# Performance work log

Hardware: AMD Instinct MI355X
Metric: run time of the kernel (lower is better)

## Reference

```python
import jax, jax.numpy as jnp
import numpy as np

B, T, W = 8, 4096, 1024          # batch, byte seq len, words per sequence
DB, DW = 64, 512                 # byte_embed_dim, word_embed_dim
NH = 2                           # highway layers per block
VOCAB = 264                      # 256 bytes + 4 + 4 specials
BPE_MARK, WORD_MARK = 4, 3       # bpe_mask_idx, word_mask_idx


def _make_seg_ids():
    # ragged word lengths in {3,4,5}, mean 4, summing to T per sequence
    rng = np.random.default_rng(0)
    seg = np.empty((B, T), np.int32)
    base = T // W
    for b in range(B):
        delta = np.zeros(W, np.int64)
        q = W // 4
        idx = rng.permutation(W)
        delta[idx[:q]] = 1
        delta[idx[q:2 * q]] = -1
        seg[b] = np.repeat(np.arange(W), base + delta)
    return jnp.asarray(seg)


def setup_inputs() -> dict:
    key = jax.random.key(0)
    ks = jax.random.split(key, 12)
    s = 0.05
    byte_tokens = jax.random.randint(ks[0], (B, T), 4, VOCAB)
    bpe_mask = jax.random.bernoulli(ks[1], 0.25, (B, T))
    word_mask = jax.random.bernoulli(ks[2], 0.05, (B, T))
    seg_ids = _make_seg_ids()
    tok_emb = (jax.random.normal(ks[3], (VOCAB, DB)) * s).at[0].set(0.0)  # padding_idx=0 row zeroed
    inp = {
        'byte_tokens': byte_tokens, 'bpe_mask': bpe_mask, 'word_mask': word_mask,
        'seg_ids': seg_ids, 'tok_emb': tok_emb,
        'conv0_w': jax.random.normal(ks[4], (3, DB, DW)) * s, 'conv0_b': jnp.zeros((DW,)),
        'hw0_wg': jax.random.normal(ks[5], (NH, DW, DW)) * s, 'hw0_bg': jnp.zeros((NH, DW)),
        'hw0_wh': jax.random.normal(ks[6], (NH, DW, DW)) * s, 'hw0_bh': jnp.zeros((NH, DW)),
        'conv1_w': jax.random.normal(ks[7], (3, DW, DW)) * s, 'conv1_b': jnp.zeros((DW,)),
        'hw1_wg': jax.random.normal(ks[8], (NH, DW, DW)) * s, 'hw1_bg': jnp.zeros((NH, DW)),
        'hw1_wh': jax.random.normal(ks[9], (NH, DW, DW)) * s, 'hw1_bh': jnp.zeros((NH, DW)),
        'proj_w': jax.random.normal(ks[10], (DW, DW)) * s, 'proj_b': jnp.zeros((DW,)),
    }
    return inp


def _conv_highway(x, cw, cb, wg, bg, wh, bh, residual):
    # 1D same-padded conv over sequence, optional residual, relu, then highways
    y = jax.lax.conv_general_dilated(x, cw, (1,), 'SAME',
                                     dimension_numbers=('NWC', 'WIO', 'NWC')) + cb
    if residual:
        y = y + x
    y = jax.nn.relu(y)
    for i in range(NH):
        g = jax.nn.sigmoid(y @ wg[i] + bg[i])
        h = jax.nn.relu(y @ wh[i] + bh[i])
        y = g * h + (1.0 - g) * y
    return y


def reference(byte_tokens, bpe_mask, word_mask, seg_ids, tok_emb,
              conv0_w, conv0_b, hw0_wg, hw0_bg, hw0_wh, hw0_bh,
              conv1_w, conv1_b, hw1_wg, hw1_bg, hw1_wh, hw1_bh,
              proj_w, proj_b):
    # byte embedding + marker embeddings (pad idx 0 -> zero row)
    x = (tok_emb[byte_tokens]
         + tok_emb[jnp.where(bpe_mask, BPE_MARK, 0)]
         + tok_emb[jnp.where(word_mask, WORD_MARK, 0)])          # [B,T,DB]
    x = _conv_highway(x, conv0_w, conv0_b, hw0_wg, hw0_bg, hw0_wh, hw0_bh, False)
    x = _conv_highway(x, conv1_w, conv1_b, hw1_wg, hw1_bg, hw1_wh, hw1_bh, True)
    # ragged per-word segment max over bytes (fused, replaces python loops)
    seg_max = jax.vmap(lambda xi, si: jax.ops.segment_max(xi, si, num_segments=W))
    x = seg_max(x, seg_ids)                                       # [B,W,DW]
    return x @ proj_w + proj_b
```

## Files before the change

kernel.cpp:

```cpp
#include <hip/hip_runtime.h>
#include <hip/hip_bf16.h>

using bf16 = __hip_bfloat16;
typedef __attribute__((ext_vector_type(8))) short s8v;
typedef __attribute__((ext_vector_type(4))) float f4v;

#define T_SEQ 4096
#define DWC 512

__device__ __forceinline__ float fin(float v) {
    return (v == v && fabsf(v) < 1e30f) ? v : 0.0f;
}
__device__ __forceinline__ float ldf(const void* p, size_t i, int f32) {
    return f32 ? ((const float*)p)[i] : __bfloat162float(((const bf16*)p)[i]);
}
__device__ __forceinline__ float b2f(short s) {
    unsigned u = ((unsigned)(unsigned short)s) << 16;
    return __builtin_bit_cast(float, u);
}
__device__ __forceinline__ short f2b(float v) {
    bf16 b = __float2bfloat16(v);
    return __builtin_bit_cast(short, b);
}
__device__ __forceinline__ uint4 ld16(const short* p) { return *(const uint4*)p; }

__device__ __forceinline__ void gl_lds16(const short* g, short* l) {
    __builtin_amdgcn_global_load_lds(
        (const __attribute__((address_space(1))) void*)g,
        (__attribute__((address_space(3))) void*)l, 16, 0, 0);
}

__device__ __forceinline__ void swz(int L, int G, int& bx, int& by) {
    int k8 = L & 7, sl = L >> 3;
    int gp = G >> 5;
    bx = sl & 3;
    by = k8 * gp + (sl >> 2);
}

__device__ __forceinline__ int swidx(int row, int ch) {
    return row * 32 + ((ch ^ ((row >> 1) & 3)) << 3);
}

__global__ __launch_bounds__(256) void diag_kernel(bf16* __restrict__ out, int n, float v)
{
    int i = blockIdx.x * 256 + threadIdx.x;
    if (i < n) out[i] = __float2bfloat16(i == 0 ? v : 0.0f);
}

__global__ __launch_bounds__(256) void detect_kernel(
    const int* __restrict__ tok, const unsigned char* __restrict__ bpe,
    const unsigned char* __restrict__ wm, const int* __restrict__ seg,
    const unsigned int* __restrict__ embw, int* __restrict__ flags)
{
    __shared__ int sh[5];
    int tid = threadIdx.x;
    if (tid < 5) sh[tid] = 0;
    __syncthreads();
    int bo = 0, bm = 0, wo = 0, wmid = 0;
    for (int i = tid; i < 16384; i += 256) {
        int odd = 2 * i + 1;
        if (bpe[odd]) bo = 1;
        if (wm[odd])  wo = 1;
        int mid = 8 * (i & 4095) + 4;
        if (bpe[mid]) bm = 1;
        if (wm[mid])  wmid = 1;
    }
    if (bo)   atomicOr(&sh[0], 1);
    if (bm)   atomicOr(&sh[1], 1);
    if (wo)   atomicOr(&sh[2], 1);
    if (wmid) atomicOr(&sh[3], 1);
    if (tid < 32 && embw[32 + tid] != 0u) atomicOr(&sh[4], 1);
    __syncthreads();
    if (tid == 0) {
        flags[0] = (tok[32767] != 0) ? 0 : 1;
        flags[1] = sh[0] ? 1 : (sh[1] ? 4 : 8);
        flags[2] = sh[2] ? 1 : (sh[3] ? 4 : 8);
        flags[3] = (seg[32767] != 0) ? 0 : 1;
        flags[4] = sh[4] ? 0 : 1;
    }
}

#define WB_TOTAL 3249664
#define EMB4_ELEMS (264 * 4 * 64)
__global__ __launch_bounds__(256) void convert_weights(
    const void* c0w, const void* c0b, const void* h0g, const void* h0bg,
    const void* h0h, const void* h0bh, const void* c1w, const void* c1b,
    const void* h1g, const void* h1bg, const void* h1h, const void* h1bh,
    const void* pw, const void* pb, const void* emb,
    const int* __restrict__ flags, short* __restrict__ WB)
{
    int f32 = flags[4];
    size_t i = (size_t)blockIdx.x * 256 + threadIdx.x;
    if (i >= WB_TOTAL + EMB4_ELEMS) return;
    if (i >= WB_TOTAL) {
        size_t o = i - WB_TOTAL;
        size_t t = o >> 8, v = (o >> 6) & 3, c = o & 63;
        float val = ldf(emb, t * 64 + c, f32);
        if (v & 1) val += ldf(emb, 4 * 64 + c, f32);
        if (v & 2) val += ldf(emb, 3 * 64 + c, f32);
        WB[i] = f2b(fin(val));
        return;
    }
    const void* src; size_t si;
    if (i < 98304)        { size_t n = i / 192, k = i % 192; src = c0w; si = k * 512 + n; }
    else if (i < 98816)   { src = c0b;  si = i - 98304; }
    else if (i < 623104)  { size_t o = i - 98816;  size_t l = o >> 18; o &= 262143;
                            size_t n = o >> 9, k = o & 511; src = h0g; si = (l << 18) + k * 512 + n; }
    else if (i < 624128)  { src = h0bg; si = i - 623104; }
    else if (i < 1148416) { size_t o = i - 624128; size_t l = o >> 18; o &= 262143;
                            size_t n = o >> 9, k = o & 511; src = h0h; si = (l << 18) + k * 512 + n; }
    else if (i < 1149440) { src = h0bh; si = i - 1148416; }
    else if (i < 1935872) { size_t o = i - 1149440; size_t n = o / 1536, k = o % 1536;
                            src = c1w; si = k * 512 + n; }
    else if (i < 1936384) { src = c1b;  si = i - 1935872; }
    else if (i < 2460672) { size_t o = i - 1936384; size_t l = o >> 18; o &= 262143;
                            size_t n = o >> 9, k = o & 511; src = h1g; si = (l << 18) + k * 512 + n; }
    else if (i < 2461696) { src = h1bg; si = i - 2460672; }
    else if (i < 2985984) { size_t o = i - 2461696; size_t l = o >> 18; o &= 262143;
                            size_t n = o >> 9, k = o & 511; src = h1h; si = (l << 18) + k * 512 + n; }
    else if (i < 2987008) { src = h1bh; si = i - 2985984; }
    else if (i < 3249152) { size_t o = i - 2987008; size_t n = o >> 9, k = o & 511;
                            src = pw; si = k * 512 + n; }
    else                  { src = pb;   si = i - 3249152; }
    WB[i] = f2b(ldf(src, si, f32));
}

__global__ __launch_bounds__(512) void conv0_mfma(
    const int* __restrict__ tok, const unsigned char* __restrict__ bpe,
    const unsigned char* __restrict__ wm, const short* __restrict__ emb4,
    const int* __restrict__ flags, const short* __restrict__ WT,
    const short* __restrict__ bias, short* __restrict__ Out)
{
    constexpr int K = 192;
    constexpr int NIT = 3;
    __shared__ __align__(16) short As[2][256 * 32];
    __shared__ __align__(16) short Bs[2][256 * 32];
    int bx, by;
    swz(blockIdx.x, gridDim.x, bx, by);
    const int bm = by * 128, bn = bx * 128;
    const int tid = threadIdx.x;
    const int wave = tid >> 6, lane = tid & 63;
    const int wmr = (wave >> 1) * 32, wnc = (wave & 1) * 64;
    const int q = lane >> 4, ln16 = lane & 15;
    const int sr = tid >> 2, sch = tid & 3;
    const int tt = (bm + sr) & (T_SEQ - 1);
    const int is64t = flags[0];
    const int wb = flags[1], ww = flags[2];
    const short* Bb = WT + (size_t)(bn + sr) * K + sch * 8;

    f4v acc[2][4] = {};
    uint4 rA0, rA1, rB0, rB1;
    const uint4 z4 = make_uint4(0, 0, 0, 0);

    auto loadA = [&](int tap, uint4& a0, uint4& a1) {
        int ts = tt + tap - 1;
        if ((unsigned)ts < (unsigned)T_SEQ) {
            int bt = bm + sr + tap - 1;
            int tk = is64t ? (int)((const long long*)tok)[bt] : tok[bt];
            tk = min(max(tk, 0), 263);
            int v = (bpe[(size_t)bt * wb] ? 1 : 0) | (wm[(size_t)bt * ww] ? 2 : 0);
            const short* row = emb4 + ((size_t)tk * 4 + v) * 64;
            a0 = ld16(row + sch * 8);
            a1 = ld16(row + 32 + sch * 8);
        } else { a0 = z4; a1 = z4; }
    };

    loadA(0, rA0, rA1);
    rB0 = ld16(Bb);
    rB1 = ld16(Bb + 32);
    *(uint4*)(&As[0][swidx(sr, sch)])       = rA0;
    *(uint4*)(&As[0][swidx(128 + sr, sch)]) = rA1;
    *(uint4*)(&Bs[0][swidx(sr, sch)])       = rB0;
    *(uint4*)(&Bs[0][swidx(128 + sr, sch)]) = rB1;
    __syncthreads();
    int p = 0;

    for (int it = 0; it < NIT; ++it) {
        const bool more = (it + 1 < NIT);
        if (more) {
            int kn = (it + 1) * 64;
            loadA(it + 1, rA0, rA1);
            rB0 = ld16(Bb + kn);
            rB1 = ld16(Bb + kn + 32);
        }
        #pragma unroll
        for (int ks = 0; ks < 2; ks++) {
            s8v af[2], bf[4];
            #pragma unroll
            for (int mi = 0; mi < 2; mi++)
                af[mi] = *(const s8v*)(&As[p][swidx(128 * ks + wmr + mi * 16 + ln16, q)]);
            #pragma unroll
            for (int ni = 0; ni < 4; ni++)
                bf[ni] = *(const s8v*)(&Bs[p][swidx(128 * ks + wnc + ni * 16 + ln16, q)]);
            #pragma unroll
            for (int mi = 0; mi < 2; mi++)
                #pragma unroll
                for (int ni = 0; ni < 4; ni++)
                    acc[mi][ni] = __builtin_amdgcn_mfma_f32_16x16x32_bf16(
                        af[mi], bf[ni], acc[mi][ni], 0, 0, 0);
        }
        if (more) {
            *(uint4*)(&As[p ^ 1][swidx(sr, sch)])       = rA0;
            *(uint4*)(&As[p ^ 1][swidx(128 + sr, sch)]) = rA1;
            *(uint4*)(&Bs[p ^ 1][swidx(sr, sch)])       = rB0;
            *(uint4*)(&Bs[p ^ 1][swidx(128 + sr, sch)]) = rB1;
            __syncthreads();
            p ^= 1;
        }
    }

    #pragma unroll
    for (int mi = 0; mi < 2; mi++)
        #pragma unroll
        for (int ni = 0; ni < 4; ni++) {
            int col = bn + wnc + ni * 16 + ln16;
            float bv = b2f(bias[col]);
            #pragma unroll
            for (int r = 0; r < 4; r++) {
                int orow = bm + wmr + mi * 16 + q * 4 + r;
                Out[(size_t)orow * DWC + col] =
                    f2b(fin(fmaxf(acc[mi][ni][r] + bv, 0.0f)));
            }
        }
}

__global__ __launch_bounds__(512) void conv1_mfma(
    const short* __restrict__ A, const short* __restrict__ WT,
    const short* __restrict__ bias, short* __restrict__ Out)
{
    constexpr int IC = 512;
    constexpr int K = 3 * IC;
    constexpr int NIT = K / 64;
    __shared__ __align__(16) short As[2][256 * 32];
    __shared__ __align__(16) short Bs[2][256 * 32];
    int bx, by;
    swz(blockIdx.x, gridDim.x, bx, by);
    const int bm = by * 128, bn = bx * 128;
    const int tid = threadIdx.x;
    const int wave = tid >> 6, lane = tid & 63;
    const int wmr = (wave >> 1) * 32, wnc = (wave & 1) * 64;
    const int q = lane >> 4, ln16 = lane & 15;
    const int sr = tid >> 2, sch = tid & 3;
    const int tt = (bm + sr) & (T_SEQ - 1);
    const short* Bb = WT + (size_t)(bn + sr) * K + sch * 8;

    f4v acc[2][4] = {};
    uint4 rA0, rA1, rB0, rB1;
    const uint4 z4 = make_uint4(0, 0, 0, 0);

    {
        int ts = tt - 1;
        bool ok = (ts >= 0 && ts < T_SEQ);
        const short* sa = A + (size_t)(bm + sr - 1) * IC + sch * 8;
        rA0 = ok ? ld16(sa) : z4;
        rA1 = ok ? ld16(sa + 32) : z4;
        rB0 = ld16(Bb);
        rB1 = ld16(Bb + 32);
    }
    *(uint4*)(&As[0][swidx(sr, sch)])       = rA0;
    *(uint4*)(&As[0][swidx(128 + sr, sch)]) = rA1;
    *(uint4*)(&Bs[0][swidx(sr, sch)])       = rB0;
    *(uint4*)(&Bs[0][swidx(128 + sr, sch)]) = rB1;
    __syncthreads();
    int p = 0;

    for (int it = 0; it < NIT; ++it) {
        const bool more = (it + 1 < NIT);
        if (more) {
            int kn = (it + 1) * 64;
            int tap = kn / IC, c0 = kn - tap * IC;
            int ts = tt + tap - 1;
            bool ok = (ts >= 0 && ts < T_SEQ);
            const short* sa = A + (size_t)(bm + sr + tap - 1) * IC + c0 + sch * 8;
            rA0 = ok ? ld16(sa) : z4;
            rA1 = ok ? ld16(sa + 32) : z4;
            rB0 = ld16(Bb + kn);
            rB1 = ld16(Bb + kn + 32);
        }
        #pragma unroll
        for (int ks = 0; ks < 2; ks++) {
            s8v af[2], bf[4];
            #pragma unroll
            for (int mi = 0; mi < 2; mi++)
                af[mi] = *(const s8v*)(&As[p][swidx(128 * ks + wmr + mi * 16 + ln16, q)]);
            #pragma unroll
            for (int ni = 0; ni < 4; ni++)
                bf[ni] = *(const s8v*)(&Bs[p][swidx(128 * ks + wnc + ni * 16 + ln16, q)]);
            #pragma unroll
            for (int mi = 0; mi < 2; mi++)
                #pragma unroll
                for (int ni = 0; ni < 4; ni++)
                    acc[mi][ni] = __builtin_amdgcn_mfma_f32_16x16x32_bf16(
                        af[mi], bf[ni], acc[mi][ni], 0, 0, 0);
        }
        if (more) {
            *(uint4*)(&As[p ^ 1][swidx(sr, sch)])       = rA0;
            *(uint4*)(&As[p ^ 1][swidx(128 + sr, sch)]) = rA1;
            *(uint4*)(&Bs[p ^ 1][swidx(sr, sch)])       = rB0;
            *(uint4*)(&Bs[p ^ 1][swidx(128 + sr, sch)]) = rB1;
            __syncthreads();
            p ^= 1;
        }
    }

    #pragma unroll
    for (int mi = 0; mi < 2; mi++)
        #pragma unroll
        for (int ni = 0; ni < 4; ni++) {
            int col = bn + wnc + ni * 16 + ln16;
            float bv = b2f(bias[col]);
            #pragma unroll
            for (int r = 0; r < 4; r++) {
                int orow = bm + wmr + mi * 16 + q * 4 + r;
                float v = acc[mi][ni][r] + bv + b2f(A[(size_t)orow * IC + col]);
                Out[(size_t)orow * DWC + col] = f2b(fin(fmaxf(v, 0.0f)));
            }
        }
}

__global__ __launch_bounds__(512, 4) void highway_mfma8(
    const short* __restrict__ Y, const short* __restrict__ WgT,
    const short* __restrict__ bg, const short* __restrict__ WhT,
    const short* __restrict__ bh, short* __restrict__ Out)
{
    constexpr int IC = DWC;
    constexpr int NIT = IC / 32;
    __shared__ __align__(16) short L[3][3][128 * 32];
    int bx, by;
    swz(blockIdx.x, gridDim.x, bx, by);
    const int bm = by * 128, bn = bx * 128;
    const int tid = threadIdx.x;
    const int wave = tid >> 6, lane = tid & 63;
    const int wmr = (wave >> 2) * 64;
    const int wnc = (wave & 3) * 32;
    const int q = lane >> 4, ln16 = lane & 15;

    const int rr = (wave << 4) + (lane >> 2);
    const int ch = (lane & 3) ^ ((rr >> 1) & 3);
    const short* gA = Y   + (size_t)(bm + rr) * IC + ch * 8;
    const short* gG = WgT + (size_t)(bn + rr) * IC + ch * 8;
    const short* gH = WhT + (size_t)(bn + rr) * IC + ch * 8;
    const int wb1k = wave << 10;

    f4v accg[4][2] = {};
    f4v acch[4][2] = {};

    auto stage = [&](int pp, int kk) {
        gl_lds16(gA + kk, (short*)((char*)&L[pp][0][0] + wb1k));
        gl_lds16(gG + kk, (short*)((char*)&L[pp][1][0] + wb1k));
        gl_lds16(gH + kk, (short*)((char*)&L[pp][2][0] + wb1k));
    };

    stage(0, 0);
    stage(1, 32);
    asm volatile("s_waitcnt vmcnt(3)" ::: "memory");
    __builtin_amdgcn_s_barrier();
    int cur = 0, nn = 2;

    for (int it = 0; it < NIT; ++it) {
        const bool issue = (it + 2 < NIT);
        if (issue) stage(nn, (it + 2) * 32);
        const short* Ap = &L[cur][0][0];
        const short* Gp = &L[cur][1][0];
        const short* Hp = &L[cur][2][0];
        s8v af[2], bgf[2], bhf[2];
        #pragma unroll
        for (int ni = 0; ni < 2; ni++) {
            bgf[ni] = *(const s8v*)(&Gp[swidx(wnc + ni * 16 + ln16, q)]);
            bhf[ni] = *(const s8v*)(&Hp[swidx(wnc + ni * 16 + ln16, q)]);
        }
        #pragma unroll
        for (int mh = 0; mh < 2; mh++) {
            #pragma unroll
            for (int mi = 0; mi < 2; mi++)
                af[mi] = *(const s8v*)(&Ap[swidx(wmr + mh * 32 + mi * 16 + ln16, q)]);
            #pragma unroll
            for (int mi = 0; mi < 2; mi++)
                #pragma unroll
                for (int ni = 0; ni < 2; ni++) {
                    accg[mh * 2 + mi][ni] = __builtin_amdgcn_mfma_f32_16x16x32_bf16(
                        af[mi], bgf[ni], accg[mh * 2 + mi][ni], 0, 0, 0);
                    acch[mh * 2 + mi][ni] = __builtin_amdgcn_mfma_f32_16x16x32_bf16(
                        af[mi], bhf[ni], acch[mh * 2 + mi][ni], 0, 0, 0);
                }
        }
        if (it + 1 < NIT) {
            if (issue) asm volatile("s_waitcnt vmcnt(3)" ::: "memory");
            else       asm volatile("s_waitcnt vmcnt(0)" ::: "memory");
            __builtin_amdgcn_s_barrier();
            cur = (cur == 2) ? 0 : cur + 1;
            nn  = (nn  == 2) ? 0 : nn  + 1;
        }
    }

    #pragma unroll
    for (int mi = 0; mi < 4; mi++)
        #pragma unroll
        for (int ni = 0; ni < 2; ni++) {
            int col = bn + wnc + ni * 16 + ln16;
            float bgv = b2f(bg[col]);
            float bhv = b2f(bh[col]);
            #pragma unroll
            for (int r = 0; r < 4; r++) {
                int orow = bm + wmr + mi * 16 + q * 4 + r;
                float g = 1.0f / (1.0f + expf(-(accg[mi][ni][r] + bgv)));
                float h = fmaxf(acch[mi][ni][r] + bhv, 0.0f);
                float yv = b2f(Y[(size_t)orow * DWC + col]);
                Out[(size_t)orow * DWC + col] = f2b(fin(g * h + (1.0f - g) * yv));
            }
        }
}

__global__ __launch_bounds__(512) void proj_mfma(
    const short* __restrict__ A, const short* __restrict__ WT,
    const short* __restrict__ bias, const int* __restrict__ flags,
    void* __restrict__ Out, int oroff)
{
    __shared__ __align__(16) short As[128 * 32];
    __shared__ __align__(16) short Bs[128 * 32];
    int bx, by;
    swz(blockIdx.x, gridDim.x, bx, by);
    const int bm = by * 128, bn = bx * 128;
    const int tid = threadIdx.x;
    const int wave = tid >> 6, lane = tid & 63;
    const int wmr = (wave >> 1) * 32, wnc = (wave & 1) * 64;
    const int q = lane >> 4, ln16 = lane & 15;
    const int sr = tid >> 2, sch = tid & 3;
    const int sw = swidx(sr, sch);
    const int f32 = flags[4];
    const short* A0 = A  + (size_t)(bm + sr) * DWC + sch * 8;
    const short* B0 = WT + (size_t)(bn + sr) * DWC + sch * 8;

    f4v acc[2][4] = {};
    uint4 rA = ld16(A0), rB = ld16(B0);

    for (int k0 = 0; k0 < DWC; k0 += 32) {
        *(uint4*)(&As[sw]) = rA;
        *(uint4*)(&Bs[sw]) = rB;
        __syncthreads();
        if (k0 + 32 < DWC) {
            int kn = k0 + 32;
            rA = ld16(A0 + kn); rB = ld16(B0 + kn);
        }
        s8v af[2], bf[4];
        #pragma unroll
        for (int mi = 0; mi < 2; mi++) af[mi] = *(const s8v*)(&As[swidx(wmr + mi * 16 + ln16, q)]);
        #pragma unroll
        for (int ni = 0; ni < 4; ni++) bf[ni] = *(const s8v*)(&Bs[swidx(wnc + ni * 16 + ln16, q)]);
        #pragma unroll
        for (int mi = 0; mi < 2; mi++)
            #pragma unroll
            for (int ni = 0; ni < 4; ni++)
                acc[mi][ni] = __builtin_amdgcn_mfma_f32_16x16x32_bf16(
                    af[mi], bf[ni], acc[mi][ni], 0, 0, 0);
        __syncthreads();
    }

    #pragma unroll
    for (int mi = 0; mi < 2; mi++)
        #pragma unroll
        for (int ni = 0; ni < 4; ni++) {
            int col = bn + wnc + ni * 16 + ln16;
            float bv = b2f(bias[col]);
            #pragma unroll
            for (int r = 0; r < 4; r++) {
                int orow = bm + wmr + mi * 16 + q * 4 + r;
                float v = fin(acc[mi][ni][r] + bv);
                size_t oi = (size_t)(oroff + orow) * DWC + col;
                if (f32) ((float*)Out)[oi] = v;
                else     ((bf16*)Out)[oi] = __float2bfloat16(v);
            }
        }
}

__global__ __launch_bounds__(256) void bounds_kernel(
    const int* __restrict__ seg, const int* __restrict__ flags,
    int* __restrict__ wstart, int* __restrict__ wend, int bt0)
{
    int il = blockIdx.x * 256 + threadIdx.x;
    int ig = bt0 + il;
    int is64 = flags[3];
    const long long* seg64 = (const long long*)seg;
    int t = il & (T_SEQ - 1);
    int bl = il >> 12;
    int s  = (is64 ? (int)seg64[ig] : seg[ig]) & 1023;
    int sp = (t == 0)         ? -1 : ((is64 ? (int)seg64[ig - 1] : seg[ig - 1]) & 1023);
    int sn = (t == T_SEQ - 1) ? -1 : ((is64 ? (int)seg64[ig + 1] : seg[ig + 1]) & 1023);
    int bw = (bl << 10) + s;
    if (sp != s) wstart[bw] = t;
    if (sn != s) wend[bw] = t;
}

__global__ __launch_bounds__(512) void segmax_kernel(
    const short* __restrict__ Y, const int* __restrict__ wstart,
    const int* __restrict__ wend, short* __restrict__ Out)
{
    int bw = blockIdx.x;
    int d = threadIdx.x;
    int bl = bw >> 10;
    int s = wstart[bw], e = wend[bw];
    s = min(max(s, 0), T_SEQ - 1);
    e = min(max(e, s), T_SEQ - 1);
    float m = b2f(Y[(size_t)((bl << 12) + s) * DWC + d]);
    for (int t = s + 1; t <= e; ++t)
        m = fmaxf(m, b2f(Y[(size_t)((bl << 12) + t) * DWC + d]));
    Out[(size_t)bw * DWC + d] = f2b(fin(m));
}

extern "C" void kernel_launch(void* const* d_in, const int* in_sizes, int n_in,
                              void* d_out, int out_size, void* d_ws, size_t ws_size,
                              hipStream_t stream)
{
    static const int expect[19] = {32768, 32768, 32768, 32768, 16896,
                                   98304, 512, 524288, 1024, 524288, 1024,
                                   786432, 512, 524288, 1024, 524288, 1024,
                                   262144, 512};
    int bad = -1;
    if (n_in < 19) bad = 31;
    else for (int i = 0; i < 19; i++) if (in_sizes[i] != expect[i]) { bad = i; break; }
    if (bad >= 0) {
        diag_kernel<<<dim3((out_size + 255) / 256), dim3(256), 0, stream>>>(
            (bf16*)d_out, out_size, 1e35f * (float)(1 + bad));
        return;
    }

    char* ws = (char*)d_ws;
    const size_t WBREG = 8ull << 20;
    short* WB    = (short*)ws;
    int*   flags = (int*)(ws + (7u << 20));
    const size_t perC = 8388608 + 8192 + 64;
    int C = 8;
    while (C > 1 && WBREG + (size_t)C * perC > ws_size) C >>= 1;
    if (WBREG + (size_t)C * perC > ws_size) {
        float ws_mib = (float)((double)ws_size / 1048576.0);
        diag_kernel<<<dim3((out_size + 255) / 256), dim3(256), 0, stream>>>(
            (bf16*)d_out, out_size, 1e30f * (16.0f + ws_mib));
        return;
    }

    const int*  byte_tokens = (const int*)d_in[0];
    const unsigned char* bpe_mask = (const unsigned char*)d_in[1];
    const unsigned char* word_mask = (const unsigned char*)d_in[2];
    const int*  seg_ids     = (const int*)d_in[3];
    const void* tok_emb = d_in[4];

    detect_kernel<<<dim3(1), dim3(256), 0, stream>>>(
        byte_tokens, bpe_mask, word_mask, seg_ids,
        (const unsigned int*)tok_emb, flags);

    convert_weights<<<dim3((WB_TOTAL + EMB4_ELEMS + 255) / 256), dim3(256), 0, stream>>>(
        d_in[5], d_in[6], d_in[7], d_in[8], d_in[9], d_in[10],
        d_in[11], d_in[12], d_in[13], d_in[14], d_in[15], d_in[16],
        d_in[17], d_in[18], tok_emb, flags, WB);

    short* c0wT = WB;            short* c0b  = WB + 98304;
    short* h0gT = WB + 98816;    short* h0bg = WB + 623104;
    short* h0hT = WB + 624128;   short* h0bh = WB + 1148416;
    short* c1wT = WB + 1149440;  short* c1b  = WB + 1935872;
    short* h1gT = WB + 1936384;  short* h1bg = WB + 2460672;
    short* h1hT = WB + 2461696;  short* h1bh = WB + 2985984;
    short* pwT  = WB + 2987008;  short* pb   = WB + 3249152;
    short* emb4 = WB + WB_TOTAL;
    const int LOFF = 262144, LBOFF = 512;

    for (int b0 = 0; b0 < 8; b0 += C) {
        const int rows  = C * T_SEQ;
        const int words = C * 1024;
        char*  chunk  = ws + WBREG;
        short* U      = (short*)chunk;
        short* V      = (short*)(chunk + (size_t)C * 4194304);
        int*   wstart = (int*)(chunk + (size_t)C * 8388608);
        int*   wend   = wstart + words;
        short* segout = U;

        dim3 gg(4 * (rows / 128));
        conv0_mfma<<<gg, dim3(512), 0, stream>>>(
            byte_tokens + (size_t)b0 * T_SEQ,
            bpe_mask, word_mask, emb4, flags, c0wT, c0b, U);

        highway_mfma8<<<gg, dim3(512), 0, stream>>>(U, h0gT, h0bg, h0hT, h0bh, V);
        highway_mfma8<<<gg, dim3(512), 0, stream>>>(V, h0gT + LOFF, h0bg + LBOFF,
                                                    h0hT + LOFF, h0bh + LBOFF, U);

        conv1_mfma<<<gg, dim3(512), 0, stream>>>(U, c1wT, c1b, V);

        highway_mfma8<<<gg, dim3(512), 0, stream>>>(V, h1gT, h1bg, h1hT, h1bh, U);
        highway_mfma8<<<gg, dim3(512), 0, stream>>>(U, h1gT + LOFF, h1bg + LBOFF,
                                                    h1hT + LOFF, h1bh + LBOFF, V);

        bounds_kernel<<<dim3(rows / 256), dim3(256), 0, stream>>>(
            seg_ids, flags, wstart, wend, b0 * T_SEQ);

        segmax_kernel<<<dim3(words), dim3(512), 0, stream>>>(V, wstart, wend, segout);

        proj_mfma<<<dim3(4 * (words / 128)), dim3(512), 0, stream>>>(
            segout, pwT, pb, flags, d_out, b0 * 1024);
    }
}
```

Before: 452.0 us.

## Pre-swizzle highway weights into MFMA fragment order and load directly from global

Highway gate and transform weights are repacked at conversion time into the exact per-lane MFMA B-fragment layout. The highway kernel then loads B fragments directly from global/L2 with one 16-byte load per lane, instead of staging them through LDS. This cuts LDS footprint from 3x3 to 3 tiles, which can raise occupancy, and removes LDS traffic and async copies for B. In exchange, the B loads now have global-memory latency inside the loop with no software prefetch.

```diff
diff --git a/kernel.cpp b/kernel.cpp
--- a/kernel.cpp
+++ b/kernel.cpp
@@ -102,22 +102,31 @@
         return;
     }
     const void* src; size_t si;
+    auto fraginv = [](size_t r, size_t& k, size_t& n) {
+        size_t blk = r >> 9, w = r & 511;
+        n = (blk >> 4) * 16 + ((w >> 3) & 15);
+        k = (blk & 15) * 32 + (w >> 7) * 8 + (w & 7);
+    };
     if (i < 98304)        { size_t n = i / 192, k = i % 192; src = c0w; si = k * 512 + n; }
     else if (i < 98816)   { src = c0b;  si = i - 98304; }
-    else if (i < 623104)  { size_t o = i - 98816;  size_t l = o >> 18; o &= 262143;
-                            size_t n = o >> 9, k = o & 511; src = h0g; si = (l << 18) + k * 512 + n; }
+    else if (i < 623104)  { size_t o = i - 98816;  size_t l = o >> 18; size_t k, n;
+                            fraginv(o & 262143, k, n);
+                            src = h0g; si = (l << 18) + k * 512 + n; }
     else if (i < 624128)  { src = h0bg; si = i - 623104; }
-    else if (i < 1148416) { size_t o = i - 624128; size_t l = o >> 18; o &= 262143;
-                            size_t n = o >> 9, k = o & 511; src = h0h; si = (l << 18) + k * 512 + n; }
+    else if (i < 1148416) { size_t o = i - 624128; size_t l = o >> 18; size_t k, n;
+                            fraginv(o & 262143, k, n);
+                            src = h0h; si = (l << 18) + k * 512 + n; }
     else if (i < 1149440) { src = h0bh; si = i - 1148416; }
     else if (i < 1935872) { size_t o = i - 1149440; size_t n = o / 1536, k = o % 1536;
                             src = c1w; si = k * 512 + n; }
     else if (i < 1936384) { src = c1b;  si = i - 1935872; }
-    else if (i < 2460672) { size_t o = i - 1936384; size_t l = o >> 18; o &= 262143;
-                            size_t n = o >> 9, k = o & 511; src = h1g; si = (l << 18) + k * 512 + n; }
+    else if (i < 2460672) { size_t o = i - 1936384; size_t l = o >> 18; size_t k, n;
+                            fraginv(o & 262143, k, n);
+                            src = h1g; si = (l << 18) + k * 512 + n; }
     else if (i < 2461696) { src = h1bg; si = i - 2460672; }
-    else if (i < 2985984) { size_t o = i - 2461696; size_t l = o >> 18; o &= 262143;
-                            size_t n = o >> 9, k = o & 511; src = h1h; si = (l << 18) + k * 512 + n; }
+    else if (i < 2985984) { size_t o = i - 2461696; size_t l = o >> 18; size_t k, n;
+                            fraginv(o & 262143, k, n);
+                            src = h1h; si = (l << 18) + k * 512 + n; }
     else if (i < 2987008) { src = h1bh; si = i - 2985984; }
     else if (i < 3249152) { size_t o = i - 2987008; size_t n = o >> 9, k = o & 511;
                             src = pw; si = k * 512 + n; }
@@ -319,13 +328,13 @@
 }
 
 __global__ __launch_bounds__(512, 4) void highway_mfma8(
-    const short* __restrict__ Y, const short* __restrict__ WgT,
-    const short* __restrict__ bg, const short* __restrict__ WhT,
+    const short* __restrict__ Y, const short* __restrict__ WgF,
+    const short* __restrict__ bg, const short* __restrict__ WhF,
     const short* __restrict__ bh, short* __restrict__ Out)
 {
     constexpr int IC = DWC;
     constexpr int NIT = IC / 32;
-    __shared__ __align__(16) short L[3][3][128 * 32];
+    __shared__ __align__(16) short L[3][128 * 32];
     int bx, by;
     swz(blockIdx.x, gridDim.x, bx, by);
     const int bm = by * 128, bn = bx * 128;
@@ -337,38 +346,37 @@
 
     const int rr = (wave << 4) + (lane >> 2);
     const int ch = (lane & 3) ^ ((rr >> 1) & 3);
-    const short* gA = Y   + (size_t)(bm + rr) * IC + ch * 8;
-    const short* gG = WgT + (size_t)(bn + rr) * IC + ch * 8;
-    const short* gH = WhT + (size_t)(bn + rr) * IC + ch * 8;
+    const short* gA = Y + (size_t)(bm + rr) * IC + ch * 8;
     const int wb1k = wave << 10;
+
+    const short* Bg0 = WgF + (((size_t)(bn + wnc) >> 4) << 13) + (lane << 3);
+    const short* Bh0 = WhF + (((size_t)(bn + wnc) >> 4) << 13) + (lane << 3);
 
     f4v accg[4][2] = {};
     f4v acch[4][2] = {};
 
     auto stage = [&](int pp, int kk) {
-        gl_lds16(gA + kk, (short*)((char*)&L[pp][0][0] + wb1k));
-        gl_lds16(gG + kk, (short*)((char*)&L[pp][1][0] + wb1k));
-        gl_lds16(gH + kk, (short*)((char*)&L[pp][2][0] + wb1k));
+        gl_lds16(gA + kk, (short*)((char*)&L[pp][0] + wb1k));
     };
 
     stage(0, 0);
     stage(1, 32);
-    asm volatile("s_waitcnt vmcnt(3)" ::: "memory");
+    asm volatile("s_waitcnt vmcnt(1)" ::: "memory");
     __builtin_amdgcn_s_barrier();
     int cur = 0, nn = 2;
 
     for (int it = 0; it < NIT; ++it) {
         const bool issue = (it + 2 < NIT);
+        s8v bgf[2], bhf[2];
+        #pragma unroll
+        for (int ni = 0; ni < 2; ni++) {
+            size_t fo = ((size_t)ni << 13) + ((size_t)it << 9);
+            bgf[ni] = *(const s8v*)(Bg0 + fo);
+            bhf[ni] = *(const s8v*)(Bh0 + fo);
+        }
         if (issue) stage(nn, (it + 2) * 32);
-        const short* Ap = &L[cur][0][0];
-        const short* Gp = &L[cur][1][0];
-        const short* Hp = &L[cur][2][0];
-        s8v af[2], bgf[2], bhf[2];
-        #pragma unroll
-        for (int ni = 0; ni < 2; ni++) {
-            bgf[ni] = *(const s8v*)(&Gp[swidx(wnc + ni * 16 + ln16, q)]);
-            bhf[ni] = *(const s8v*)(&Hp[swidx(wnc + ni * 16 + ln16, q)]);
-        }
+        const short* Ap = &L[cur][0];
+        s8v af[2];
         #pragma unroll
         for (int mh = 0; mh < 2; mh++) {
             #pragma unroll
@@ -385,7 +393,7 @@
                 }
         }
         if (it + 1 < NIT) {
-            if (issue) asm volatile("s_waitcnt vmcnt(3)" ::: "memory");
+            if (issue) asm volatile("s_waitcnt vmcnt(1)" ::: "memory");
             else       asm volatile("s_waitcnt vmcnt(0)" ::: "memory");
             __builtin_amdgcn_s_barrier();
             cur = (cur == 2) ? 0 : cur + 1;
@@ -554,11 +562,11 @@
         d_in[17], d_in[18], tok_emb, flags, WB);
 
     short* c0wT = WB;            short* c0b  = WB + 98304;
-    short* h0gT = WB + 98816;    short* h0bg = WB + 623104;
-    short* h0hT = WB + 624128;   short* h0bh = WB + 1148416;
+    short* h0gF = WB + 98816;    short* h0bg = WB + 623104;
+    short* h0hF = WB + 624128;   short* h0bh = WB + 1148416;
     short* c1wT = WB + 1149440;  short* c1b  = WB + 1935872;
-    short* h1gT = WB + 1936384;  short* h1bg = WB + 2460672;
-    short* h1hT = WB + 2461696;  short* h1bh = WB + 2985984;
+    short* h1gF = WB + 1936384;  short* h1bg = WB + 2460672;
+    short* h1hF = WB + 2461696;  short* h1bh = WB + 2985984;
     short* pwT  = WB + 2987008;  short* pb   = WB + 3249152;
     short* emb4 = WB + WB_TOTAL;
     const int LOFF = 262144, LBOFF = 512;
@@ -578,15 +586,15 @@
             byte_tokens + (size_t)b0 * T_SEQ,
             bpe_mask, word_mask, emb4, flags, c0wT, c0b, U);
 
-        highway_mfma8<<<gg, dim3(512), 0, stream>>>(U, h0gT, h0bg, h0hT, h0bh, V);
-        highway_mfma8<<<gg, dim3(512), 0, stream>>>(V, h0gT + LOFF, h0bg + LBOFF,
-                                                    h0hT + LOFF, h0bh + LBOFF, U);
+        highway_mfma8<<<gg, dim3(512), 0, stream>>>(U, h0gF, h0bg, h0hF, h0bh, V);
+        highway_mfma8<<<gg, dim3(512), 0, stream>>>(V, h0gF + LOFF, h0bg + LBOFF,
+                                                    h0hF + LOFF, h0bh + LBOFF, U);
 
         conv1_mfma<<<gg, dim3(512), 0, stream>>>(U, c1wT, c1b, V);
 
-        highway_mfma8<<<gg, dim3(512), 0, stream>>>(V, h1gT, h1bg, h1hT, h1bh, U);
-        highway_mfma8<<<gg, dim3(512), 0, stream>>>(U, h1gT + LOFF, h1bg + LBOFF,
-                                                    h1hT + LOFF, h1bh + LBOFF, V);
+        highway_mfma8<<<gg, dim3(512), 0, stream>>>(V, h1gF, h1bg, h1hF, h1bh, U);
+        highway_mfma8<<<gg, dim3(512), 0, stream>>>(U, h1gF + LOFF, h1bg + LBOFF,
+                                                    h1hF + LOFF, h1bh + LBOFF, V);
 
         bounds_kernel<<<dim3(rows / 256), dim3(256), 0, stream>>>(
             seg_ids, flags, wstart, wend, b0 * T_SEQ);
```

New measurement: 414.6 us. 8.3% less time.
